# Kernel tuning notes

Measured on AMD Instinct MI355X. Metric: run time of the kernel, lower is better.

The kernel has to match this reference:

```python
import jax, jax.numpy as jnp
import numpy as np

D_MODEL = 1024
D_STATE = 16
D_CONV = 4
D_INNER = 2048  # expand * d_model
BATCH = 2
LENGTH = 2048


def silu(u):
    return u * jax.nn.sigmoid(u)


def setup_inputs() -> dict:
    key = jax.random.key(0)
    ks = jax.random.split(key, 8)
    sc = 0.02
    x = jax.random.normal(ks[0], (BATCH, LENGTH, D_MODEL), jnp.float32)
    W_in = jax.random.normal(ks[1], (2 * D_INNER, D_MODEL), jnp.float32) * sc
    conv_w = jax.random.normal(ks[2], (D_INNER, 1, D_CONV), jnp.float32) * 0.1
    conv_b = jnp.zeros((D_INNER,), jnp.float32)
    W_x = jax.random.normal(ks[3], (D_INNER + 2 * D_STATE, D_INNER), jnp.float32) * sc
    W_dt = jax.random.normal(ks[4], (D_INNER, D_INNER), jnp.float32) * sc
    b_dt = jnp.zeros((D_INNER,), jnp.float32)
    # A = arange(1, d_state+1) repeated for each inner channel (per source init)
    A_log = jnp.log(jnp.tile(jnp.arange(1, D_STATE + 1, dtype=jnp.float32), (D_INNER, 1)))
    D = jnp.ones((D_INNER,), jnp.float32)
    W_out = jax.random.normal(ks[5], (D_MODEL, D_INNER), jnp.float32) * sc
    ln_g = jnp.ones((D_MODEL,), jnp.float32)
    ln_b = jnp.zeros((D_MODEL,), jnp.float32)
    return dict(x=x, W_in=W_in, conv_w=conv_w, conv_b=conv_b, W_x=W_x, W_dt=W_dt,
                b_dt=b_dt, A_log=A_log, D=D, W_out=W_out, ln_g=ln_g, ln_b=ln_b)


def reference(x, W_in, conv_w, conv_b, W_x, W_dt, b_dt, A_log, D, W_out, ln_g, ln_b):
    b, l, _ = x.shape
    residual = x
    # in_proj, split into x-path and gate z
    xz = x @ W_in.T  # (b, l, 2*d_inner)
    xs, z = jnp.split(xz, 2, axis=-1)
    # depthwise causal conv1d (left pad d_conv-1, take first l outputs)
    xc = jnp.transpose(xs, (0, 2, 1))  # (b, d_inner, l)
    xc = jax.lax.conv_general_dilated(
        xc, conv_w, window_strides=(1,), padding=[(D_CONV - 1, 0)],
        dimension_numbers=('NCH', 'OIH', 'NCH'), feature_group_count=D_INNER)
    xc = xc + conv_b[None, :, None]
    u = silu(jnp.transpose(xc, (0, 2, 1)))  # (b, l, d_inner)
    # SSM parameter projection
    proj = u @ W_x.T  # (b, l, d_inner + 2*d_state)
    d_in, Bm, Cm = jnp.split(proj, [D_INNER, D_INNER + D_STATE], axis=-1)
    delta = jax.nn.softplus(d_in @ W_dt.T + b_dt)  # (b, l, d_inner)
    A = -jnp.exp(A_log)  # (d_inner, d_state)
    dA = jnp.exp(delta[..., None] * A)                         # (b, l, d, n)
    dBu = delta[..., None] * Bm[:, :, None, :] * u[..., None]  # (b, l, d, n)

    def step(state, inp):
        dA_t, dBu_t, c_t = inp
        state = state * dA_t + dBu_t            # (b, d, n)
        y_t = jnp.einsum('bdn,bn->bd', state, c_t)
        return state, y_t

    init = jnp.zeros((b, D_INNER, D_STATE), x.dtype)
    _, ys = jax.lax.scan(step, init, (jnp.transpose(dA, (1, 0, 2, 3)),
                                      jnp.transpose(dBu, (1, 0, 2, 3)),
                                      jnp.transpose(Cm, (1, 0, 2))))
    y = jnp.transpose(ys, (1, 0, 2)) + u * D  # (b, l, d_inner)
    y = y * silu(z)
    out = y @ W_out.T + residual
    mu = jnp.mean(out, axis=-1, keepdims=True)
    var = jnp.var(out, axis=-1, keepdims=True)
    return (out - mu) / jnp.sqrt(var + 1e-5) * ln_g + ln_b
```

## Files before the change

kernel.cpp:

```cpp
#include <hip/hip_runtime.h>

typedef unsigned short u16;
typedef unsigned int u32;
typedef __bf16 bf16x8_t __attribute__((ext_vector_type(8)));
typedef float f32x4_t __attribute__((ext_vector_type(4)));


#define NCH 64
#define CLEN 32

__device__ __forceinline__ u16 f2bf(float f) {
  u32 u = __float_as_uint(f);
  return (u16)((u + 0x7fffu + ((u >> 16) & 1u)) >> 16);
}
__device__ __forceinline__ float bf2f(u16 h) { return __uint_as_float(((u32)h) << 16); }

__device__ __forceinline__ void async_ld16(const u16* g, u16* l) {
  __builtin_amdgcn_global_load_lds((const __attribute__((address_space(1))) void*)g,
                                   (__attribute__((address_space(3))) void*)l, 16, 0, 0);
}

__global__ void k_cvt_all(const float* __restrict__ x, u16* __restrict__ x_bf,
                          const float* __restrict__ W_in, u16* __restrict__ Win_bf,
                          const float* __restrict__ W_x, u16* __restrict__ Wx_bf,
                          const float* __restrict__ W_dt, u16* __restrict__ Wdt_bf,
                          const float* __restrict__ W_out, u16* __restrict__ Wout_bf) {
  int g = blockIdx.x * 256 + threadIdx.x;
  const float* src;
  u16* dst;
  int rel;
  bool valid = true;
  if (g < 1048576) { src = x; dst = x_bf; rel = g; }
  else if (g < 2097152) { src = W_in; dst = Win_bf; rel = g - 1048576; }
  else if (g < 3211264) { src = W_x; dst = Wx_bf; rel = g - 2097152; valid = rel < 1064960; }
  else if (g < 4259840) { src = W_dt; dst = Wdt_bf; rel = g - 3211264; }
  else if (g < 4784128) { src = W_out; dst = Wout_bf; rel = g - 4259840; }
  else return;
  u32 lo = 0, hi = 0;
  if (valid) {
    float4 v = reinterpret_cast<const float4*>(src)[rel];
    lo = (u32)f2bf(v.x) | ((u32)f2bf(v.y) << 16);
    hi = (u32)f2bf(v.z) | ((u32)f2bf(v.w) << 16);
  }
  reinterpret_cast<uint2*>(dst)[rel] = make_uint2(lo, hi);
}

template <bool WB, bool WF, bool DB>
__global__ __launch_bounds__(256, 2) void k_gemm_bt(
    const u16* __restrict__ A, int lda, const u16* __restrict__ B, int ldb,
    float* __restrict__ Cf, int fcol0, int ldcf, size_t fsplit,
    u16* __restrict__ Cb, int ldc, int K) {
  __shared__ __align__(16) u16 sA[(DB ? 2 : 1) * 128 * 64];
  __shared__ __align__(16) u16 sB[(DB ? 2 : 1) * 128 * 64];
  const int tid = threadIdx.x;
  const int lane = tid & 63;
  const int wave = tid >> 6;
  const size_t tm = (size_t)blockIdx.y * 128;
  const size_t tn = (size_t)blockIdx.x * 128;
  const int kbase = blockIdx.z * K;
  const int wm = (wave & 1) * 64;
  const int wn = (wave >> 1) * 64;
  const int mrow = lane & 15;
  const int quad = lane >> 4;

  f32x4_t acc[4][4];
#pragma unroll
  for (int i = 0; i < 4; ++i)
#pragma unroll
    for (int j = 0; j < 4; ++j) {
      acc[i][j][0] = 0.f; acc[i][j][1] = 0.f; acc[i][j][2] = 0.f; acc[i][j][3] = 0.f;
    }

  auto stage = [&](int k0, int buf) {
#pragma unroll
    for (int j = 0; j < 4; ++j) {
      int idx = j * 256 + tid;
      int row = idx >> 3;
      int col = (idx & 7) << 3;
      async_ld16(A + (tm + row) * (size_t)lda + (kbase + k0 + col), sA + buf * 8192 + (size_t)idx * 8);
      async_ld16(B + (tn + row) * (size_t)ldb + (kbase + k0 + col), sB + buf * 8192 + (size_t)idx * 8);
    }
  };
  auto compute = [&](int buf) {
    const u16* bA = sA + buf * 8192;
    const u16* bB = sB + buf * 8192;
#pragma unroll
    for (int kk = 0; kk < 64; kk += 32) {
      bf16x8_t af[4], bfr[4];
#pragma unroll
      for (int i = 0; i < 4; ++i)
        af[i] = *reinterpret_cast<const bf16x8_t*>(bA + (wm + i * 16 + mrow) * 64 + kk + quad * 8);
#pragma unroll
      for (int i = 0; i < 4; ++i)
        bfr[i] = *reinterpret_cast<const bf16x8_t*>(bB + (wn + i * 16 + mrow) * 64 + kk + quad * 8);
#pragma unroll
      for (int i = 0; i < 4; ++i)
#pragma unroll
        for (int j = 0; j < 4; ++j)
          acc[i][j] = __builtin_amdgcn_mfma_f32_16x16x32_bf16(af[i], bfr[j], acc[i][j], 0, 0, 0);
    }
  };

  if (DB) {
    const int nit = K >> 6;
    stage(0, 0);
    __syncthreads();
    for (int it = 0; it < nit; ++it) {
      if (it + 1 < nit) stage((it + 1) << 6, (it + 1) & 1);
      compute(it & 1);
      __syncthreads();
    }
  } else {
    for (int k0 = 0; k0 < K; k0 += 64) {
      stage(k0, 0);
      __syncthreads();
      compute(0);
      __syncthreads();
    }
  }

  if (WF) Cf += (size_t)blockIdx.z * fsplit;
#pragma unroll
  for (int i = 0; i < 4; ++i)
#pragma unroll
    for (int j = 0; j < 4; ++j) {
      size_t r0 = tm + wm + i * 16 + quad * 4;
      size_t c = tn + wn + j * 16 + mrow;
#pragma unroll
      for (int r = 0; r < 4; ++r) {
        float v = acc[i][j][r];
        if (WF && (int)c >= fcol0) Cf[(r0 + r) * (size_t)ldcf + (c - fcol0)] = v;
        if (WB) Cb[(r0 + r) * (size_t)ldc + c] = f2bf(v);
      }
    }
}

__global__ void k_conv_silu(const u16* __restrict__ xz, const float* __restrict__ cw,
                            const float* __restrict__ cb, u16* __restrict__ u) {
  int g = blockIdx.x * 256 + threadIdx.x;
  int d = g & 2047;
  int l = (g >> 11) & 2047;
  int b = g >> 22;
  float acc = cb[d];
#pragma unroll
  for (int k = 0; k < 4; ++k) {
    int lp = l + k - 3;
    if (lp >= 0) acc += bf2f(xz[((size_t)(b * 2048 + lp) << 12) + d]) * cw[d * 4 + k];
  }
  float s = acc / (1.f + __expf(-acc));
  u[g] = f2bf(s);
}

__device__ __forceinline__ float softplus_fast(float x) {
  return __logf(1.f + __expf(x));
}

__global__ void k_scan1(const u16* __restrict__ dpre, const float* __restrict__ bdt,
                        const u16* __restrict__ u, const float* __restrict__ projBC,
                        const float* __restrict__ A_log, float* __restrict__ sF,
                        float* __restrict__ aF) {
  int d = blockIdx.x * 256 + threadIdx.x;
  int c = blockIdx.y, b = blockIdx.z;
  float A[16], s[16], ap[16];
#pragma unroll
  for (int q = 0; q < 4; ++q) {
    float4 al = reinterpret_cast<const float4*>(A_log + d * 16)[q];
    A[q * 4 + 0] = -__expf(al.x); A[q * 4 + 1] = -__expf(al.y);
    A[q * 4 + 2] = -__expf(al.z); A[q * 4 + 3] = -__expf(al.w);
  }
#pragma unroll
  for (int n = 0; n < 16; ++n) { s[n] = 0.f; ap[n] = 1.f; }
  float bd = bdt[d];
  int t0 = c * CLEN;
  for (int t = t0; t < t0 + CLEN; ++t) {
    size_t rb = (size_t)(b * 2048 + t);
    float delta = softplus_fast(bf2f(dpre[rb * 2048 + d]) + bd);
    float du = delta * bf2f(u[rb * 2048 + d]);
    const float4* Bp = reinterpret_cast<const float4*>(projBC + rb * 128);
    float4 B0 = Bp[0], B1 = Bp[1], B2 = Bp[2], B3 = Bp[3];
    float Bv[16] = {B0.x, B0.y, B0.z, B0.w, B1.x, B1.y, B1.z, B1.w,
                    B2.x, B2.y, B2.z, B2.w, B3.x, B3.y, B3.z, B3.w};
#pragma unroll
    for (int n = 0; n < 16; ++n) {
      float dA = __expf(delta * A[n]);
      s[n] = fmaf(s[n], dA, du * Bv[n]);
      ap[n] *= dA;
    }
  }
  size_t o = ((size_t)((b * NCH + c) * 2048 + d)) << 4;
#pragma unroll
  for (int q = 0; q < 4; ++q) {
    reinterpret_cast<float4*>(sF + o)[q] = make_float4(s[q * 4], s[q * 4 + 1], s[q * 4 + 2], s[q * 4 + 3]);
    reinterpret_cast<float4*>(aF + o)[q] = make_float4(ap[q * 4], ap[q * 4 + 1], ap[q * 4 + 2], ap[q * 4 + 3]);
  }
}

__global__ void k_scan_carry(const float* __restrict__ sF, const float* __restrict__ aF,
                             float* __restrict__ carry) {
  int g = blockIdx.x * 256 + threadIdx.x;
  int b = g >> 15;
  int dn = g & 32767;
  float S = 0.f;
#pragma unroll 4
  for (int c = 0; c < NCH; ++c) {
    size_t idx = ((size_t)(b * NCH + c) << 15) + dn;
    carry[idx] = S;
    S = S * aF[idx] + sF[idx];
  }
}

__global__ void k_scan3(const u16* __restrict__ dpre, const float* __restrict__ bdt,
                        const u16* __restrict__ u, const float* __restrict__ projBC,
                        const float* __restrict__ A_log, const float* __restrict__ carry,
                        const float* __restrict__ Dvec, const u16* __restrict__ xz,
                        u16* __restrict__ ybf) {
  int d = blockIdx.x * 256 + threadIdx.x;
  int c = blockIdx.y, b = blockIdx.z;
  float A[16], s[16];
#pragma unroll
  for (int q = 0; q < 4; ++q) {
    float4 al = reinterpret_cast<const float4*>(A_log + d * 16)[q];
    A[q * 4 + 0] = -__expf(al.x); A[q * 4 + 1] = -__expf(al.y);
    A[q * 4 + 2] = -__expf(al.z); A[q * 4 + 3] = -__expf(al.w);
  }
  size_t o = ((size_t)((b * NCH + c) * 2048 + d)) << 4;
#pragma unroll
  for (int q = 0; q < 4; ++q) {
    float4 cv = reinterpret_cast<const float4*>(carry + o)[q];
    s[q * 4] = cv.x; s[q * 4 + 1] = cv.y; s[q * 4 + 2] = cv.z; s[q * 4 + 3] = cv.w;
  }
  float bd = bdt[d];
  float Dd = Dvec[d];
  int t0 = c * CLEN;
  for (int t = t0; t < t0 + CLEN; ++t) {
    size_t rb = (size_t)(b * 2048 + t);
    float delta = softplus_fast(bf2f(dpre[rb * 2048 + d]) + bd);
    float uv = bf2f(u[rb * 2048 + d]);
    float du = delta * uv;
    const float4* Bp = reinterpret_cast<const float4*>(projBC + rb * 128);
    float4 B0 = Bp[0], B1 = Bp[1], B2 = Bp[2], B3 = Bp[3];
    float4 C0 = Bp[4], C1 = Bp[5], C2 = Bp[6], C3 = Bp[7];
    float Bv[16] = {B0.x, B0.y, B0.z, B0.w, B1.x, B1.y, B1.z, B1.w,
                    B2.x, B2.y, B2.z, B2.w, B3.x, B3.y, B3.z, B3.w};
    float Cv[16] = {C0.x, C0.y, C0.z, C0.w, C1.x, C1.y, C1.z, C1.w,
                    C2.x, C2.y, C2.z, C2.w, C3.x, C3.y, C3.z, C3.w};
    float yv = 0.f;
#pragma unroll
    for (int n = 0; n < 16; ++n) {
      float dA = __expf(delta * A[n]);
      s[n] = fmaf(s[n], dA, du * Bv[n]);
      yv = fmaf(s[n], Cv[n], yv);
    }
    yv += uv * Dd;
    float z = bf2f(xz[(rb << 12) + 2048 + d]);
    yv *= z / (1.f + __expf(-z));
    ybf[rb * 2048 + d] = f2bf(yv);
  }
}

__global__ void k_ln(const float* __restrict__ pre, const float* __restrict__ x,
                     const float* __restrict__ gam, const float* __restrict__ bet,
                     float* __restrict__ out) {
  int row = blockIdx.x, tid = threadIdx.x;
  size_t base = (size_t)row * 1024 + tid * 4;
  float4 v = *reinterpret_cast<const float4*>(pre + base);
  float4 p1 = *reinterpret_cast<const float4*>(pre + 4194304 + base);
  float4 r = *reinterpret_cast<const float4*>(x + base);
  v.x += p1.x + r.x; v.y += p1.y + r.y; v.z += p1.z + r.z; v.w += p1.w + r.w;
  float s = v.x + v.y + v.z + v.w;
  float s2 = v.x * v.x + v.y * v.y + v.z * v.z + v.w * v.w;
#pragma unroll
  for (int o = 32; o >= 1; o >>= 1) {
    s += __shfl_xor(s, o);
    s2 += __shfl_xor(s2, o);
  }
  __shared__ float red[8];
  int lane = tid & 63, wv = tid >> 6;
  if (lane == 0) { red[wv] = s; red[4 + wv] = s2; }
  __syncthreads();
  s = red[0] + red[1] + red[2] + red[3];
  s2 = red[4] + red[5] + red[6] + red[7];
  float mu = s * (1.f / 1024.f);
  float var = s2 * (1.f / 1024.f) - mu * mu;
  float rstd = rsqrtf(var + 1e-5f);
  float4 gg = *reinterpret_cast<const float4*>(gam + tid * 4);
  float4 bb = *reinterpret_cast<const float4*>(bet + tid * 4);
  float4 o;
  o.x = (v.x - mu) * rstd * gg.x + bb.x;
  o.y = (v.y - mu) * rstd * gg.y + bb.y;
  o.z = (v.z - mu) * rstd * gg.z + bb.z;
  o.w = (v.w - mu) * rstd * gg.w + bb.w;
  *reinterpret_cast<float4*>(out + base) = o;
}

extern "C" void kernel_launch(void* const* d_in, const int* in_sizes, int n_in,
                              void* d_out, int out_size, void* d_ws, size_t ws_size,
                              hipStream_t stream) {
  (void)in_sizes; (void)n_in; (void)out_size; (void)ws_size;
  const float* x = (const float*)d_in[0];
  const float* W_in = (const float*)d_in[1];
  const float* conv_w = (const float*)d_in[2];
  const float* conv_b = (const float*)d_in[3];
  const float* W_x = (const float*)d_in[4];
  const float* W_dt = (const float*)d_in[5];
  const float* b_dt = (const float*)d_in[6];
  const float* A_log = (const float*)d_in[7];
  const float* Dv = (const float*)d_in[8];
  const float* W_out = (const float*)d_in[9];
  const float* ln_g = (const float*)d_in[10];
  const float* ln_b = (const float*)d_in[11];
  float* out = (float*)d_out;

  char* p = (char*)d_ws;
  u16* xz_bf = (u16*)p;      p += (size_t)4096 * 4096 * 2;
  u16* u_bf = (u16*)p;       p += (size_t)4096 * 2048 * 2;
  float* projBC = (float*)p; p += (size_t)4096 * 128 * 4;
  u16* projbf = (u16*)p;     p += (size_t)4096 * 2176 * 2;
  u16* dpre_bf = (u16*)p;    p += (size_t)4096 * 2048 * 2;
  u16* ybf = (u16*)p;        p += (size_t)4096 * 2048 * 2;
  float* sF = (float*)p;     p += (size_t)2 * NCH * 2048 * 16 * 4;
  float* aF = (float*)p;     p += (size_t)2 * NCH * 2048 * 16 * 4;
  float* carry = (float*)p;  p += (size_t)2 * NCH * 2048 * 16 * 4;
  u16* Wx_bf = (u16*)p;      p += (size_t)2176 * 2048 * 2;
  u16* Wdt_bf = (u16*)p;     p += (size_t)2048 * 2048 * 2;
  u16* Wout_bf = (u16*)p;    p += (size_t)1024 * 2048 * 2;
  u16* x_bf = (u16*)p;       p += (size_t)4096 * 1024 * 2;
  u16* Win_bf = (u16*)p;     p += (size_t)4096 * 1024 * 2;
  float* outpre = sF;

  k_cvt_all<<<18688, 256, 0, stream>>>(x, x_bf, W_in, Win_bf, W_x, Wx_bf, W_dt, Wdt_bf,
                                       W_out, Wout_bf);

  k_gemm_bt<true, false, false><<<dim3(32, 32), 256, 0, stream>>>(
      x_bf, 1024, Win_bf, 1024, nullptr, 0, 0, 0, xz_bf, 4096, 1024);
  k_conv_silu<<<32768, 256, 0, stream>>>(xz_bf, conv_w, conv_b, u_bf);
  k_gemm_bt<true, true, true><<<dim3(17, 32), 256, 0, stream>>>(
      u_bf, 2048, Wx_bf, 2048, projBC, 2048, 128, 0, projbf, 2176, 2048);
  k_gemm_bt<true, false, true><<<dim3(16, 32), 256, 0, stream>>>(
      projbf, 2176, Wdt_bf, 2048, nullptr, 0, 0, 0, dpre_bf, 2048, 2048);
  k_scan1<<<dim3(8, NCH, 2), 256, 0, stream>>>(dpre_bf, b_dt, u_bf, projBC, A_log, sF, aF);
  k_scan_carry<<<256, 256, 0, stream>>>(sF, aF, carry);
  k_scan3<<<dim3(8, NCH, 2), 256, 0, stream>>>(dpre_bf, b_dt, u_bf, projBC, A_log, carry,
                                               Dv, xz_bf, ybf);
  k_gemm_bt<false, true, true><<<dim3(8, 32, 2), 256, 0, stream>>>(
      ybf, 2048, Wout_bf, 2048, outpre, 0, 1024, (size_t)4096 * 1024, nullptr, 0, 1024);
  k_ln<<<4096, 256, 0, stream>>>(outpre, x, ln_g, ln_b, out);
}
```

Measured before the change: 483.2 us.

## Fold W_dt into W_x to fuse dt projection and split-K the B/C projection

Precomputes Weff = W_dt · W_x[:2048] (via a transpose and a small GEMM) so the dt pre-activation comes from a single u·Weff GEMM. This removes the 4096x2176x2048 projection GEMM and its bf16 intermediate. The B/C columns get their own split-K GEMM with a reduce kernel, and conv_silu is vectorized to 8 channels per thread. The GEMM double-buffering path is dropped, and the weight product is recomputed every call in bf16, which changes rounding relative to the reference.

New measurement: 453.3 us. 1.07x faster.

```diff
diff --git a/kernel.cpp b/kernel.cpp
--- a/kernel.cpp
+++ b/kernel.cpp
@@ -45,13 +45,40 @@
   reinterpret_cast<uint2*>(dst)[rel] = make_uint2(lo, hi);
 }
 
-template <bool WB, bool WF, bool DB>
+__global__ void k_transpose(const u16* __restrict__ in, u16* __restrict__ out) {
+  __shared__ u16 tile[64][72];
+  int bx = blockIdx.x;
+  int by = blockIdx.y;
+  int t = threadIdx.x;
+#pragma unroll
+  for (int i = 0; i < 2; ++i) {
+    int idx = i * 256 + t;
+    int r = idx >> 3;
+    int c = (idx & 7) * 8;
+    *reinterpret_cast<uint4*>(&tile[r][c]) =
+        *reinterpret_cast<const uint4*>(in + (size_t)(by * 64 + r) * 2048 + bx * 64 + c);
+  }
+  __syncthreads();
+#pragma unroll
+  for (int i = 0; i < 2; ++i) {
+    int idx = i * 256 + t;
+    int r = idx >> 3;
+    int c = (idx & 7) * 8;
+    u16 tmp[8];
+#pragma unroll
+    for (int e = 0; e < 8; ++e) tmp[e] = tile[c + e][r];
+    *reinterpret_cast<uint4*>(out + (size_t)(bx * 64 + r) * 2048 + by * 64 + c) =
+        *reinterpret_cast<uint4*>(tmp);
+  }
+}
+
+template <bool WB, bool WF>
 __global__ __launch_bounds__(256, 2) void k_gemm_bt(
     const u16* __restrict__ A, int lda, const u16* __restrict__ B, int ldb,
-    float* __restrict__ Cf, int fcol0, int ldcf, size_t fsplit,
+    float* __restrict__ Cf, int ldcf, size_t fsplit,
     u16* __restrict__ Cb, int ldc, int K) {
-  __shared__ __align__(16) u16 sA[(DB ? 2 : 1) * 128 * 64];
-  __shared__ __align__(16) u16 sB[(DB ? 2 : 1) * 128 * 64];
+  __shared__ __align__(16) u16 sA[128 * 64];
+  __shared__ __align__(16) u16 sB[128 * 64];
   const int tid = threadIdx.x;
   const int lane = tid & 63;
   const int wave = tid >> 6;
@@ -71,52 +98,32 @@
       acc[i][j][0] = 0.f; acc[i][j][1] = 0.f; acc[i][j][2] = 0.f; acc[i][j][3] = 0.f;
     }
 
-  auto stage = [&](int k0, int buf) {
+  for (int k0 = 0; k0 < K; k0 += 64) {
 #pragma unroll
     for (int j = 0; j < 4; ++j) {
       int idx = j * 256 + tid;
       int row = idx >> 3;
       int col = (idx & 7) << 3;
-      async_ld16(A + (tm + row) * (size_t)lda + (kbase + k0 + col), sA + buf * 8192 + (size_t)idx * 8);
-      async_ld16(B + (tn + row) * (size_t)ldb + (kbase + k0 + col), sB + buf * 8192 + (size_t)idx * 8);
-    }
-  };
-  auto compute = [&](int buf) {
-    const u16* bA = sA + buf * 8192;
-    const u16* bB = sB + buf * 8192;
+      async_ld16(A + (tm + row) * (size_t)lda + (kbase + k0 + col), sA + (size_t)idx * 8);
+      async_ld16(B + (tn + row) * (size_t)ldb + (kbase + k0 + col), sB + (size_t)idx * 8);
+    }
+    __syncthreads();
 #pragma unroll
     for (int kk = 0; kk < 64; kk += 32) {
       bf16x8_t af[4], bfr[4];
 #pragma unroll
       for (int i = 0; i < 4; ++i)
-        af[i] = *reinterpret_cast<const bf16x8_t*>(bA + (wm + i * 16 + mrow) * 64 + kk + quad * 8);
+        af[i] = *reinterpret_cast<const bf16x8_t*>(sA + (wm + i * 16 + mrow) * 64 + kk + quad * 8);
 #pragma unroll
       for (int i = 0; i < 4; ++i)
-        bfr[i] = *reinterpret_cast<const bf16x8_t*>(bB + (wn + i * 16 + mrow) * 64 + kk + quad * 8);
+        bfr[i] = *reinterpret_cast<const bf16x8_t*>(sB + (wn + i * 16 + mrow) * 64 + kk + quad * 8);
 #pragma unroll
       for (int i = 0; i < 4; ++i)
 #pragma unroll
         for (int j = 0; j < 4; ++j)
           acc[i][j] = __builtin_amdgcn_mfma_f32_16x16x32_bf16(af[i], bfr[j], acc[i][j], 0, 0, 0);
     }
-  };
-
-  if (DB) {
-    const int nit = K >> 6;
-    stage(0, 0);
     __syncthreads();
-    for (int it = 0; it < nit; ++it) {
-      if (it + 1 < nit) stage((it + 1) << 6, (it + 1) & 1);
-      compute(it & 1);
-      __syncthreads();
-    }
-  } else {
-    for (int k0 = 0; k0 < K; k0 += 64) {
-      stage(k0, 0);
-      __syncthreads();
-      compute(0);
-      __syncthreads();
-    }
   }
 
   if (WF) Cf += (size_t)blockIdx.z * fsplit;
@@ -129,26 +136,58 @@
 #pragma unroll
       for (int r = 0; r < 4; ++r) {
         float v = acc[i][j][r];
-        if (WF && (int)c >= fcol0) Cf[(r0 + r) * (size_t)ldcf + (c - fcol0)] = v;
+        if (WF) Cf[(r0 + r) * (size_t)ldcf + c] = v;
         if (WB) Cb[(r0 + r) * (size_t)ldc + c] = f2bf(v);
       }
     }
 }
 
+__global__ void k_bc_reduce(const float* __restrict__ part, float* __restrict__ projBC) {
+  int g = blockIdx.x * 256 + threadIdx.x;
+  int r = g >> 3, c4 = (g & 7) * 4;
+  size_t idx = (size_t)r * 128 + c4;
+  float4 a = *reinterpret_cast<const float4*>(part + idx);
+  float4 b = *reinterpret_cast<const float4*>(part + 524288 + idx);
+  float4 c = *reinterpret_cast<const float4*>(part + 1048576 + idx);
+  float4 d = *reinterpret_cast<const float4*>(part + 1572864 + idx);
+  float4 o;
+  o.x = a.x + b.x + c.x + d.x;
+  o.y = a.y + b.y + c.y + d.y;
+  o.z = a.z + b.z + c.z + d.z;
+  o.w = a.w + b.w + c.w + d.w;
+  *reinterpret_cast<float4*>(projBC + idx) = o;
+}
+
 __global__ void k_conv_silu(const u16* __restrict__ xz, const float* __restrict__ cw,
                             const float* __restrict__ cb, u16* __restrict__ u) {
-  int g = blockIdx.x * 256 + threadIdx.x;
-  int d = g & 2047;
-  int l = (g >> 11) & 2047;
-  int b = g >> 22;
-  float acc = cb[d];
+  int bl = blockIdx.x;
+  int l = bl & 2047;
+  int d0 = threadIdx.x * 8;
+  float acc[8];
+  float4 cb0 = *reinterpret_cast<const float4*>(cb + d0);
+  float4 cb1 = *reinterpret_cast<const float4*>(cb + d0 + 4);
+  acc[0] = cb0.x; acc[1] = cb0.y; acc[2] = cb0.z; acc[3] = cb0.w;
+  acc[4] = cb1.x; acc[5] = cb1.y; acc[6] = cb1.z; acc[7] = cb1.w;
+  float4 w[8];
+#pragma unroll
+  for (int i = 0; i < 8; ++i) w[i] = *reinterpret_cast<const float4*>(cw + (d0 + i) * 4);
 #pragma unroll
   for (int k = 0; k < 4; ++k) {
     int lp = l + k - 3;
-    if (lp >= 0) acc += bf2f(xz[((size_t)(b * 2048 + lp) << 12) + d]) * cw[d * 4 + k];
-  }
-  float s = acc / (1.f + __expf(-acc));
-  u[g] = f2bf(s);
+    if (lp >= 0) {
+      bf16x8_t xv = *reinterpret_cast<const bf16x8_t*>(xz + ((size_t)(bl + k - 3) << 12) + d0);
+#pragma unroll
+      for (int i = 0; i < 8; ++i)
+        acc[i] += (float)xv[i] * reinterpret_cast<const float*>(&w[i])[k];
+    }
+  }
+  u16 tmp[8];
+#pragma unroll
+  for (int i = 0; i < 8; ++i) {
+    float s = acc[i] / (1.f + __expf(-acc[i]));
+    tmp[i] = f2bf(s);
+  }
+  *reinterpret_cast<uint4*>(u + ((size_t)bl << 11) + d0) = *reinterpret_cast<uint4*>(tmp);
 }
 
 __device__ __forceinline__ float softplus_fast(float x) {
@@ -315,34 +354,40 @@
   u16* xz_bf = (u16*)p;      p += (size_t)4096 * 4096 * 2;
   u16* u_bf = (u16*)p;       p += (size_t)4096 * 2048 * 2;
   float* projBC = (float*)p; p += (size_t)4096 * 128 * 4;
-  u16* projbf = (u16*)p;     p += (size_t)4096 * 2176 * 2;
   u16* dpre_bf = (u16*)p;    p += (size_t)4096 * 2048 * 2;
   u16* ybf = (u16*)p;        p += (size_t)4096 * 2048 * 2;
   float* sF = (float*)p;     p += (size_t)2 * NCH * 2048 * 16 * 4;
   float* aF = (float*)p;     p += (size_t)2 * NCH * 2048 * 16 * 4;
   float* carry = (float*)p;  p += (size_t)2 * NCH * 2048 * 16 * 4;
   u16* Wx_bf = (u16*)p;      p += (size_t)2176 * 2048 * 2;
+  u16* WxT_bf = (u16*)p;     p += (size_t)2048 * 2048 * 2;
+  u16* Weff_bf = (u16*)p;    p += (size_t)2048 * 2048 * 2;
   u16* Wdt_bf = (u16*)p;     p += (size_t)2048 * 2048 * 2;
   u16* Wout_bf = (u16*)p;    p += (size_t)1024 * 2048 * 2;
   u16* x_bf = (u16*)p;       p += (size_t)4096 * 1024 * 2;
   u16* Win_bf = (u16*)p;     p += (size_t)4096 * 1024 * 2;
+  float* BCpart = sF;
   float* outpre = sF;
 
   k_cvt_all<<<18688, 256, 0, stream>>>(x, x_bf, W_in, Win_bf, W_x, Wx_bf, W_dt, Wdt_bf,
                                        W_out, Wout_bf);
-
-  k_gemm_bt<true, false, false><<<dim3(32, 32), 256, 0, stream>>>(
-      x_bf, 1024, Win_bf, 1024, nullptr, 0, 0, 0, xz_bf, 4096, 1024);
-  k_conv_silu<<<32768, 256, 0, stream>>>(xz_bf, conv_w, conv_b, u_bf);
-  k_gemm_bt<true, true, true><<<dim3(17, 32), 256, 0, stream>>>(
-      u_bf, 2048, Wx_bf, 2048, projBC, 2048, 128, 0, projbf, 2176, 2048);
-  k_gemm_bt<true, false, true><<<dim3(16, 32), 256, 0, stream>>>(
-      projbf, 2176, Wdt_bf, 2048, nullptr, 0, 0, 0, dpre_bf, 2048, 2048);
+  k_transpose<<<dim3(32, 32), 256, 0, stream>>>(Wx_bf, WxT_bf);
+  k_gemm_bt<true, false><<<dim3(16, 16), 256, 0, stream>>>(
+      Wdt_bf, 2048, WxT_bf, 2048, nullptr, 0, 0, Weff_bf, 2048, 2048);
+  k_gemm_bt<true, false><<<dim3(32, 32), 256, 0, stream>>>(
+      x_bf, 1024, Win_bf, 1024, nullptr, 0, 0, xz_bf, 4096, 1024);
+  k_conv_silu<<<4096, 256, 0, stream>>>(xz_bf, conv_w, conv_b, u_bf);
+  k_gemm_bt<false, true><<<dim3(1, 32, 4), 256, 0, stream>>>(
+      u_bf, 2048, Wx_bf + (size_t)2048 * 2048, 2048, BCpart, 128, (size_t)4096 * 128,
+      nullptr, 0, 512);
+  k_bc_reduce<<<128, 256, 0, stream>>>(BCpart, projBC);
+  k_gemm_bt<true, false><<<dim3(16, 32), 256, 0, stream>>>(
+      u_bf, 2048, Weff_bf, 2048, nullptr, 0, 0, dpre_bf, 2048, 2048);
   k_scan1<<<dim3(8, NCH, 2), 256, 0, stream>>>(dpre_bf, b_dt, u_bf, projBC, A_log, sF, aF);
   k_scan_carry<<<256, 256, 0, stream>>>(sF, aF, carry);
   k_scan3<<<dim3(8, NCH, 2), 256, 0, stream>>>(dpre_bf, b_dt, u_bf, projBC, A_log, carry,
                                                Dv, xz_bf, ybf);
-  k_gemm_bt<false, true, true><<<dim3(8, 32, 2), 256, 0, stream>>>(
-      ybf, 2048, Wout_bf, 2048, outpre, 0, 1024, (size_t)4096 * 1024, nullptr, 0, 1024);
+  k_gemm_bt<false, true><<<dim3(8, 32, 2), 256, 0, stream>>>(
+      ybf, 2048, Wout_bf, 2048, outpre, 1024, (size_t)4096 * 1024, nullptr, 0, 1024);
   k_ln<<<4096, 256, 0, stream>>>(outpre, x, ln_g, ln_b, out);
 }
```
